# Kernel optimization log

Hardware: AMD Instinct MI355X
Metric: run time of the kernel (lower is better)

Reference implementation:

```python
import jax, jax.numpy as jnp
import numpy as np

B, T, OBS, ENC, H, A = 32, 512, 256, 1024, 1024, 64
AR_COEF, TAR_COEF = 0.01, 0.01
LN_EPS = 1e-5


def setup_inputs() -> dict:
    key = jax.random.key(0)
    ks = jax.random.split(key, 8)
    s = 0.02  # weight scale to keep activations in a sane range
    # PyTorch LSTM bias init in source: zeros, forget-gate slice [H:2H] = 1.0 (both b_ih and b_hh)
    b_gate = jnp.zeros((4 * H,), jnp.float32).at[H:2 * H].set(1.0)
    return {
        "obs": jax.random.normal(ks[0], (B, T, OBS), jnp.float32),
        "hxs": jnp.zeros((B, H), jnp.float32),
        "cxs": jnp.zeros((B, H), jnp.float32),
        "W1": jax.random.normal(ks[1], (ENC, OBS), jnp.float32) * s,
        "b1": jnp.zeros((ENC,), jnp.float32),
        "W2": jax.random.normal(ks[2], (ENC, ENC), jnp.float32) * s,
        "b2": jnp.zeros((ENC,), jnp.float32),
        "W_ih": jax.random.normal(ks[3], (4 * H, ENC), jnp.float32) * s,
        "W_hh": jax.random.normal(ks[4], (4 * H, H), jnp.float32) * s,
        "b_ih": b_gate,
        "b_hh": b_gate,
        "ln_g": jnp.ones((H,), jnp.float32),
        "ln_b": jnp.zeros((H,), jnp.float32),
        "Wa": jax.random.normal(ks[5], (A, H), jnp.float32) * s,
        "ba": jnp.zeros((A,), jnp.float32),
        "Wc": jax.random.normal(ks[6], (1, H), jnp.float32) * s,
        "bc": jnp.zeros((1,), jnp.float32),
    }


def reference(obs, hxs, cxs, W1, b1, W2, b2, W_ih, W_hh, b_ih, b_hh,
              ln_g, ln_b, Wa, ba, Wc, bc):
    # Encoder: Linear -> SiLU -> Linear -> SiLU
    enc = jax.nn.silu(obs @ W1.T + b1)
    enc = jax.nn.silu(enc @ W2.T + b2)  # (B,T,ENC)

    # LSTM (WeightDrop is identity in eval mode / p=0). Precompute input gates.
    gx = enc @ W_ih.T + (b_ih + b_hh)  # (B,T,4H)

    def step(carry, g_t):
        h, c = carry
        g = g_t + h @ W_hh.T  # (B,4H), PyTorch gate order: i, f, g, o
        i, f, gc, o = jnp.split(g, 4, axis=-1)
        c = jax.nn.sigmoid(f) * c + jax.nn.sigmoid(i) * jnp.tanh(gc)
        h = jax.nn.sigmoid(o) * jnp.tanh(c)
        return (h, c), h

    (h_n, c_n), hs = jax.lax.scan(step, (hxs, cxs), jnp.swapaxes(gx, 0, 1))
    out = jnp.swapaxes(hs, 0, 1)  # (B,T,H)

    # LayerNorm
    mu = out.mean(-1, keepdims=True)
    var = out.var(-1, keepdims=True)
    out = (out - mu) / jnp.sqrt(var + LN_EPS) * ln_g + ln_b

    ar_loss = jnp.mean(out ** 2) * AR_COEF
    tar_loss = jnp.mean((out[:, 1:, :] - out[:, :-1, :]) ** 2) * TAR_COEF

    logits = out @ Wa.T + ba          # (B,T,A)
    values = (out @ Wc.T + bc)[..., 0]  # (B,T)
    return logits, values, h_n, c_n, ar_loss, tar_loss
```

## Files before the change

kernel.cpp:

```cpp
#include <hip/hip_runtime.h>


typedef _Float16 half8 __attribute__((ext_vector_type(8)));
typedef _Float16 half4v __attribute__((ext_vector_type(4)));
typedef float floatx4 __attribute__((ext_vector_type(4)));
typedef unsigned long long ull;

__device__ __forceinline__ float sigmoidf_(float x) { return 1.f / (1.f + __expf(-x)); }
__device__ __forceinline__ float tanhf_(float x) {
  x = fminf(15.f, fmaxf(-15.f, x));
  float e = __expf(-2.f * x);
  return (1.f - e) / (1.f + e);
}

__global__ __launch_bounds__(256) void k_convert_all(
    const float* s0, _Float16* d0, int n0,
    const float* s1, _Float16* d1, int n1,
    const float* s2, _Float16* d2, int n2,
    const float* s3, _Float16* d3, int n3,
    const float* s4, _Float16* d4, int n4,
    const float* s5, _Float16* d5, int n5,
    const float* s6, _Float16* d6, int n6,
    const float* s7, _Float16* d7, int n7)
{
  const int gid = blockIdx.x * 256 + threadIdx.x;
  const int stride = gridDim.x * 256;
#define CONV_SEG(s, d, n)                                                  \
  for (int i = gid; i < (n); i += stride) {                                \
    floatx4 v = *(const floatx4*)((s) + (size_t)i * 4);                    \
    half4v h;                                                              \
    h[0] = (_Float16)v[0]; h[1] = (_Float16)v[1];                          \
    h[2] = (_Float16)v[2]; h[3] = (_Float16)v[3];                          \
    *(half4v*)((d) + (size_t)i * 4) = h;                                   \
  }
  CONV_SEG(s0, d0, n0)
  CONV_SEG(s1, d1, n1)
  CONV_SEG(s2, d2, n2)
  CONV_SEG(s3, d3, n3)
  CONV_SEG(s4, d4, n4)
  CONV_SEG(s5, d5, n5)
  CONV_SEG(s6, d6, n6)
  CONV_SEG(s7, d7, n7)
#undef CONV_SEG
}

template<int EPI>
__global__ __launch_bounds__(256) void k_gemm(
    const _Float16* __restrict__ A, const _Float16* __restrict__ B,
    _Float16* __restrict__ C, const float* __restrict__ bias0,
    const float* __restrict__ bias1, int M, int N, int K)
{
  __shared__ _Float16 As[128 * 32];
  __shared__ _Float16 Bs[128 * 32];
  const int tid = threadIdx.x;
  const int l = tid & 63;
  const int w = tid >> 6;
  const int wr = w >> 1, wc = w & 1;
  const _Float16* Ab = A + (size_t)blockIdx.x * 128 * K;
  const _Float16* Bb = B + (size_t)blockIdx.y * 128 * K;

  floatx4 acc[4][4];
#pragma unroll
  for (int a = 0; a < 4; ++a)
#pragma unroll
    for (int b = 0; b < 4; ++b) acc[a][b] = (floatx4){0.f, 0.f, 0.f, 0.f};

  const int ci0 = tid, ci1 = tid + 256;
  const int r0 = ci0 >> 2, r1 = ci1 >> 2;
  const int q0 = (ci0 & 3) ^ ((r0 >> 2) & 3);
  const int q1 = (ci1 & 3) ^ ((r1 >> 2) & 3);
  const int lr = l & 15;
  const int ko = l >> 4;
  const int nkt = K >> 5;

  for (int kt = 0; kt < nkt; ++kt) {
    const _Float16* Ak = Ab + kt * 32;
    const _Float16* Bk = Bb + kt * 32;
    uint4 va0 = *(const uint4*)(Ak + (size_t)r0 * K + q0 * 8);
    uint4 va1 = *(const uint4*)(Ak + (size_t)r1 * K + q1 * 8);
    uint4 vb0 = *(const uint4*)(Bk + (size_t)r0 * K + q0 * 8);
    uint4 vb1 = *(const uint4*)(Bk + (size_t)r1 * K + q1 * 8);
    __syncthreads();
    *(uint4*)(As + ci0 * 8) = va0;
    *(uint4*)(As + ci1 * 8) = va1;
    *(uint4*)(Bs + ci0 * 8) = vb0;
    *(uint4*)(Bs + ci1 * 8) = vb1;
    __syncthreads();
    half8 af[4], bf[4];
#pragma unroll
    for (int mr = 0; mr < 4; ++mr) {
      int row = wr * 64 + mr * 16 + lr;
      int cq = ko ^ ((row >> 2) & 3);
      af[mr] = *(const half8*)(As + row * 32 + cq * 8);
    }
#pragma unroll
    for (int nc = 0; nc < 4; ++nc) {
      int col = wc * 64 + nc * 16 + lr;
      int cq = ko ^ ((col >> 2) & 3);
      bf[nc] = *(const half8*)(Bs + col * 32 + cq * 8);
    }
#pragma unroll
    for (int mr = 0; mr < 4; ++mr)
#pragma unroll
      for (int nc = 0; nc < 4; ++nc)
        acc[mr][nc] = __builtin_amdgcn_mfma_f32_16x16x32_f16(af[mr], bf[nc], acc[mr][nc], 0, 0, 0);
  }

  const int lq = l >> 4;
#pragma unroll
  for (int nc = 0; nc < 4; ++nc) {
    int gcol = blockIdx.y * 128 + wc * 64 + nc * 16 + lr;
    float bia = bias0[gcol];
    if (EPI == 1) bia += bias1[gcol];
#pragma unroll
    for (int mr = 0; mr < 4; ++mr) {
      int grow = blockIdx.x * 128 + wr * 64 + mr * 16 + lq * 4;
#pragma unroll
      for (int i = 0; i < 4; ++i) {
        float v = acc[mr][nc][i] + bia;
        if (EPI == 0) v = v * sigmoidf_(v);
        C[(size_t)(grow + i) * N + gcol] = (_Float16)v;
      }
    }
  }
}

__global__ __launch_bounds__(256, 1) void k_scan(
    const _Float16* __restrict__ gx,
    const _Float16* __restrict__ Whh,
    const float* __restrict__ cxs,
    _Float16* __restrict__ hstate,
    int* __restrict__ flags,
    _Float16* __restrict__ outh,
    float* __restrict__ out_hn, float* __restrict__ out_cn)
{
  const int blk = blockIdx.x;
  const int hbase = blk * 16;
  const int tid = threadIdx.x, l = tid & 63, wq = tid >> 6;
  __shared__ float red[2][4][4][2][4][64];

  const int cc = l & 15, ko = l >> 4;

  half8 bfr[4][8];
#pragma unroll
  for (int q = 0; q < 4; ++q)
#pragma unroll
    for (int kk = 0; kk < 8; ++kk)
      bfr[q][kk] = *(const half8*)(Whh + (size_t)(q * 1024 + hbase + cc) * 1024
                                   + wq * 256 + kk * 32 + ko * 8);

  const int gb = tid >> 3, gc2 = tid & 7;
  float c0 = cxs[gb * 1024 + hbase + gc2 * 2 + 0];
  float c1 = cxs[gb * 1024 + hbase + gc2 * 2 + 1];
  const int gmt = gb >> 4, greg = gb & 3;
  const int lane0 = ((gb & 15) >> 2) * 16 + gc2 * 2;

  const int* myflag = flags + ((wq * 16 + (l & 15)) * 4 + (l >> 4)) * 16;
  int* ourflag = flags + (blk * 4 + wq) * 16;

  unsigned gxv[4];
#pragma unroll
  for (int q = 0; q < 4; ++q)
    gxv[q] = *(const unsigned*)(gx + (size_t)gb * 512 * 4096
                                + q * 1024 + hbase + gc2 * 2);

  for (int t = 0; t < 512; ++t) {
    if (t > 0) {
      int guard = 0;
      while (true) {
        int f = __hip_atomic_load(myflag, __ATOMIC_RELAXED, __HIP_MEMORY_SCOPE_AGENT);
        if (__all(f >= t)) break;
        if (++guard > (1 << 17)) break;
        __builtin_amdgcn_s_sleep(1);
      }
      asm volatile("" ::: "memory");
      __builtin_amdgcn_sched_barrier(0);
    }

    const _Float16* hcur = hstate + (size_t)(t & 1) * 32768;
    const ull* p0 = (const ull*)(hcur + cc * 1024 + wq * 256 + ko * 8);
    const ull* p1 = (const ull*)(hcur + (16 + cc) * 1024 + wq * 256 + ko * 8);
    ull ld0[16], ld1[16];
#pragma unroll
    for (int kk = 0; kk < 8; ++kk) {
      ld0[kk * 2 + 0] = __hip_atomic_load(p0 + kk * 8 + 0, __ATOMIC_RELAXED, __HIP_MEMORY_SCOPE_AGENT);
      ld0[kk * 2 + 1] = __hip_atomic_load(p0 + kk * 8 + 1, __ATOMIC_RELAXED, __HIP_MEMORY_SCOPE_AGENT);
      ld1[kk * 2 + 0] = __hip_atomic_load(p1 + kk * 8 + 0, __ATOMIC_RELAXED, __HIP_MEMORY_SCOPE_AGENT);
      ld1[kk * 2 + 1] = __hip_atomic_load(p1 + kk * 8 + 1, __ATOMIC_RELAXED, __HIP_MEMORY_SCOPE_AGENT);
    }

    floatx4 acc[4][2];
#pragma unroll
    for (int q = 0; q < 4; ++q) {
      acc[q][0] = (floatx4){0.f, 0.f, 0.f, 0.f};
      acc[q][1] = (floatx4){0.f, 0.f, 0.f, 0.f};
    }
#pragma unroll
    for (int kk = 0; kk < 8; ++kk) {
      union { ull u2[2]; half8 h; } a0, a1;
      a0.u2[0] = ld0[kk * 2 + 0]; a0.u2[1] = ld0[kk * 2 + 1];
      a1.u2[0] = ld1[kk * 2 + 0]; a1.u2[1] = ld1[kk * 2 + 1];
#pragma unroll
      for (int q = 0; q < 4; ++q) {
        acc[q][0] = __builtin_amdgcn_mfma_f32_16x16x32_f16(a0.h, bfr[q][kk], acc[q][0], 0, 0, 0);
        acc[q][1] = __builtin_amdgcn_mfma_f32_16x16x32_f16(a1.h, bfr[q][kk], acc[q][1], 0, 0, 0);
      }
    }
    const int pp = t & 1;
#pragma unroll
    for (int q = 0; q < 4; ++q)
#pragma unroll
      for (int mt = 0; mt < 2; ++mt)
#pragma unroll
        for (int i = 0; i < 4; ++i)
          red[pp][wq][q][mt][i][l] = acc[q][mt][i];
    asm volatile("s_waitcnt lgkmcnt(0)" ::: "memory");
    __builtin_amdgcn_s_barrier();
    __builtin_amdgcn_sched_barrier(0);

    float pre0[4], pre1[4];
#pragma unroll
    for (int q = 0; q < 4; ++q) {
      pre0[q] = red[pp][0][q][gmt][greg][lane0] + red[pp][1][q][gmt][greg][lane0]
              + red[pp][2][q][gmt][greg][lane0] + red[pp][3][q][gmt][greg][lane0];
      pre1[q] = red[pp][0][q][gmt][greg][lane0 + 1] + red[pp][1][q][gmt][greg][lane0 + 1]
              + red[pp][2][q][gmt][greg][lane0 + 1] + red[pp][3][q][gmt][greg][lane0 + 1];
    }
    union { unsigned u; _Float16 h[2]; } g0, g1, g2, g3;
    g0.u = gxv[0]; g1.u = gxv[1]; g2.u = gxv[2]; g3.u = gxv[3];

    float i0 = sigmoidf_(pre0[0] + (float)g0.h[0]);
    float f0 = sigmoidf_(pre0[1] + (float)g1.h[0]);
    float gg0 = tanhf_(pre0[2] + (float)g2.h[0]);
    float o0 = sigmoidf_(pre0[3] + (float)g3.h[0]);
    c0 = f0 * c0 + i0 * gg0;
    float h0 = o0 * tanhf_(c0);

    float i1 = sigmoidf_(pre1[0] + (float)g0.h[1]);
    float f1 = sigmoidf_(pre1[1] + (float)g1.h[1]);
    float gg1 = tanhf_(pre1[2] + (float)g2.h[1]);
    float o1 = sigmoidf_(pre1[3] + (float)g3.h[1]);
    c1 = f1 * c1 + i1 * gg1;
    float h1 = o1 * tanhf_(c1);

    union { _Float16 h[2]; unsigned u; } hp;
    hp.h[0] = (_Float16)h0; hp.h[1] = (_Float16)h1;

    __hip_atomic_store((unsigned*)(hstate + (size_t)((t + 1) & 1) * 32768
                                   + (size_t)gb * 1024 + hbase + gc2 * 2),
                       hp.u, __ATOMIC_RELAXED, __HIP_MEMORY_SCOPE_AGENT);
    asm volatile("s_waitcnt vmcnt(0)" ::: "memory");
    __builtin_amdgcn_sched_barrier(0);
    if (l == 0 && t < 511)
      __hip_atomic_store(ourflag, t + 1, __ATOMIC_RELAXED,
                         __HIP_MEMORY_SCOPE_AGENT);

    *(unsigned*)(outh + ((size_t)gb * 512 + t) * 1024 + hbase + gc2 * 2) = hp.u;
    if (t == 511) {
      float2 hv; hv.x = h0; hv.y = h1;
      float2 cv; cv.x = c0; cv.y = c1;
      *(float2*)(out_hn + gb * 1024 + hbase + gc2 * 2) = hv;
      *(float2*)(out_cn + gb * 1024 + hbase + gc2 * 2) = cv;
    } else {
#pragma unroll
      for (int q = 0; q < 4; ++q)
        gxv[q] = *(const unsigned*)(gx + ((size_t)gb * 512 + t + 1) * 4096
                                    + q * 1024 + hbase + gc2 * 2);
    }
    __builtin_amdgcn_sched_barrier(0);
  }
}

__global__ __launch_bounds__(256) void k_ln(
    const _Float16* __restrict__ x, const float* __restrict__ gam,
    const float* __restrict__ bet, _Float16* __restrict__ y,
    float* __restrict__ arpart)
{
  const int m = blockIdx.x;
  const int tid = threadIdx.x;
  const int w = tid >> 6, l = tid & 63;
  half4v v = *(const half4v*)(x + (size_t)m * 1024 + tid * 4);
  float xv[4]; float s = 0.f, ss = 0.f;
#pragma unroll
  for (int j = 0; j < 4; ++j) { xv[j] = (float)v[j]; s += xv[j]; ss += xv[j] * xv[j]; }
#pragma unroll
  for (int off = 32; off > 0; off >>= 1) { s += __shfl_xor(s, off, 64); ss += __shfl_xor(ss, off, 64); }
  __shared__ float sw[4], ssw[4], bcast[2];
  if (l == 0) { sw[w] = s; ssw[w] = ss; }
  __syncthreads();
  if (tid == 0) {
    float S = sw[0] + sw[1] + sw[2] + sw[3];
    float SS = ssw[0] + ssw[1] + ssw[2] + ssw[3];
    float mu = S * (1.f / 1024.f);
    float var = SS * (1.f / 1024.f) - mu * mu;
    bcast[0] = mu; bcast[1] = rsqrtf(var + 1e-5f);
  }
  __syncthreads();
  float mu = bcast[0], rstd = bcast[1];
  float part = 0.f; half4v o;
#pragma unroll
  for (int j = 0; j < 4; ++j) {
    float nv = (xv[j] - mu) * rstd * gam[tid * 4 + j] + bet[tid * 4 + j];
    o[j] = (_Float16)nv;
    part += nv * nv;
  }
  *(half4v*)(y + (size_t)m * 1024 + tid * 4) = o;
#pragma unroll
  for (int off = 32; off > 0; off >>= 1) part += __shfl_xor(part, off, 64);
  if (l == 0) sw[w] = part;
  __syncthreads();
  if (tid == 0) arpart[m] = sw[0] + sw[1] + sw[2] + sw[3];
}

__global__ __launch_bounds__(256) void k_tar(const _Float16* __restrict__ y, float* __restrict__ tarpart) {
  const int tid = threadIdx.x;
  int gid = blockIdx.x * 256 + tid;
  const int stride = gridDim.x * 256;
  const int TOT = 32 * 511 * 256;
  float s = 0.f;
  for (int v = gid; v < TOT; v += stride) {
    int b = v / (511 * 256);
    int r = v - b * (511 * 256);
    size_t base = (size_t)b * 512 * 1024 + (size_t)r * 4;
    half4v a = *(const half4v*)(y + base);
    half4v c = *(const half4v*)(y + base + 1024);
#pragma unroll
    for (int j = 0; j < 4; ++j) { float d = (float)c[j] - (float)a[j]; s += d * d; }
  }
#pragma unroll
  for (int off = 32; off > 0; off >>= 1) s += __shfl_xor(s, off, 64);
  __shared__ float sw[4];
  if ((tid & 63) == 0) sw[tid >> 6] = s;
  __syncthreads();
  if (tid == 0) tarpart[blockIdx.x] = sw[0] + sw[1] + sw[2] + sw[3];
}

__global__ __launch_bounds__(256) void k_reduce(
    const float* __restrict__ arpart, const float* __restrict__ tarpart,
    float* __restrict__ dst)
{
  const int tid = threadIdx.x;
  float a = 0.f, t = 0.f;
  for (int i = tid; i < 16384; i += 256) a += arpart[i];
  for (int i = tid; i < 2048; i += 256) t += tarpart[i];
#pragma unroll
  for (int off = 32; off > 0; off >>= 1) { a += __shfl_xor(a, off, 64); t += __shfl_xor(t, off, 64); }
  __shared__ float sa[4], st[4];
  if ((tid & 63) == 0) { sa[tid >> 6] = a; st[tid >> 6] = t; }
  __syncthreads();
  if (tid == 0) {
    dst[0] = (sa[0] + sa[1] + sa[2] + sa[3]) * (0.01f / 16777216.f);
    dst[1] = (st[0] + st[1] + st[2] + st[3]) * (0.01f / 16744448.f);
  }
}

__global__ __launch_bounds__(256) void k_logits(
    const _Float16* __restrict__ X, const _Float16* __restrict__ Wa,
    const float* __restrict__ ba, float* __restrict__ out)
{
  const int tid = threadIdx.x, l = tid & 63, w = tid >> 6;
  const int lr = l & 15, lq = l >> 4;
  const int rowb = blockIdx.x * 64 + w * 16;
  floatx4 acc[4];
#pragma unroll
  for (int nc = 0; nc < 4; ++nc) acc[nc] = (floatx4){0.f, 0.f, 0.f, 0.f};
  for (int kc = 0; kc < 32; ++kc) {
    int k = kc * 32 + lq * 8;
    half8 af = *(const half8*)(X + (size_t)(rowb + lr) * 1024 + k);
#pragma unroll
    for (int nc = 0; nc < 4; ++nc) {
      half8 bf = *(const half8*)(Wa + (size_t)(nc * 16 + lr) * 1024 + k);
      acc[nc] = __builtin_amdgcn_mfma_f32_16x16x32_f16(af, bf, acc[nc], 0, 0, 0);
    }
  }
#pragma unroll
  for (int nc = 0; nc < 4; ++nc) {
    int col = nc * 16 + lr;
    float bia = ba[col];
#pragma unroll
    for (int i = 0; i < 4; ++i) {
      int grow = rowb + lq * 4 + i;
      out[(size_t)grow * 64 + col] = acc[nc][i] + bia;
    }
  }
}

__global__ __launch_bounds__(256) void k_values(
    const _Float16* __restrict__ X, const _Float16* __restrict__ Wc,
    const float* __restrict__ bc, float* __restrict__ out)
{
  const int tid = threadIdx.x, l = tid & 63, w = tid >> 6;
  half8 w0 = *(const half8*)(Wc + l * 16);
  half8 w1 = *(const half8*)(Wc + l * 16 + 8);
  float bias = bc[0];
  const int rowb = blockIdx.x * 64 + w * 16;
  for (int r = 0; r < 16; ++r) {
    const _Float16* xr = X + (size_t)(rowb + r) * 1024 + l * 16;
    half8 x0 = *(const half8*)(xr);
    half8 x1 = *(const half8*)(xr + 8);
    float s = 0.f;
#pragma unroll
    for (int j = 0; j < 8; ++j) s += (float)x0[j] * (float)w0[j] + (float)x1[j] * (float)w1[j];
#pragma unroll
    for (int off = 32; off > 0; off >>= 1) s += __shfl_xor(s, off, 64);
    if (l == 0) out[rowb + r] = s + bias;
  }
}

extern "C" void kernel_launch(void* const* d_in, const int* in_sizes, int n_in,
                              void* d_out, int out_size, void* d_ws, size_t ws_size,
                              hipStream_t stream)
{
  const float* obs = (const float*)d_in[0];
  const float* hxs = (const float*)d_in[1];
  const float* cxs = (const float*)d_in[2];
  const float* W1  = (const float*)d_in[3];
  const float* b1  = (const float*)d_in[4];
  const float* W2  = (const float*)d_in[5];
  const float* b2  = (const float*)d_in[6];
  const float* Wih = (const float*)d_in[7];
  const float* Whh = (const float*)d_in[8];
  const float* bih = (const float*)d_in[9];
  const float* bhh = (const float*)d_in[10];
  const float* lng = (const float*)d_in[11];
  const float* lnb = (const float*)d_in[12];
  const float* Wa  = (const float*)d_in[13];
  const float* ba  = (const float*)d_in[14];
  const float* Wc  = (const float*)d_in[15];
  const float* bc  = (const float*)d_in[16];

  char* ws = (char*)d_ws;
  size_t off = 0;
  auto alloc = [&](size_t bytes) -> char* {
    char* p = ws + off;
    off += (bytes + 255) & ~(size_t)255;
    return p;
  };
  _Float16* obs16 = (_Float16*)alloc(4194304ull * 2);
  _Float16* W1x   = (_Float16*)alloc(262144ull * 2);
  _Float16* W2x   = (_Float16*)alloc(1048576ull * 2);
  _Float16* Wihx  = (_Float16*)alloc(4194304ull * 2);
  _Float16* Whhx  = (_Float16*)alloc(4194304ull * 2);
  _Float16* Wax   = (_Float16*)alloc(65536ull * 2);
  _Float16* Wcx   = (_Float16*)alloc(1024ull * 2);
  _Float16* enc1  = (_Float16*)alloc(16384ull * 1024 * 2);
  _Float16* enc2  = (_Float16*)alloc(16384ull * 1024 * 2);
  _Float16* gx    = (_Float16*)alloc(16384ull * 4096 * 2);
  _Float16* hstate= (_Float16*)alloc(2ull * 32 * 1024 * 2);
  int* flags      = (int*)alloc(64ull * 4 * 16 * 4);
  _Float16* outh  = (_Float16*)alloc(16384ull * 1024 * 2);
  float* arpart   = (float*)alloc(16384ull * 4);
  float* tarpart  = (float*)alloc(2048ull * 4);
  _Float16* normed = enc1;

  float* out_f      = (float*)d_out;
  float* out_logits = out_f;
  float* out_values = out_f + 1048576;
  float* out_hn     = out_f + 1064960;
  float* out_cn     = out_f + 1097728;
  float* out_loss   = out_f + 1130496;

  hipMemsetAsync(flags, 0, 64ull * 4 * 16 * 4, stream);

  k_convert_all<<<2048, 256, 0, stream>>>(
      obs, obs16, 4194304 / 4,
      W1, W1x, 262144 / 4,
      W2, W2x, 1048576 / 4,
      Wih, Wihx, 4194304 / 4,
      Whh, Whhx, 4194304 / 4,
      Wa, Wax, 65536 / 4,
      Wc, Wcx, 1024 / 4,
      hxs, hstate, 32768 / 4);

  k_gemm<0><<<dim3(128, 8), 256, 0, stream>>>(obs16, W1x, enc1, b1, nullptr, 16384, 1024, 256);
  k_gemm<0><<<dim3(128, 8), 256, 0, stream>>>(enc1, W2x, enc2, b2, nullptr, 16384, 1024, 1024);
  k_gemm<1><<<dim3(128, 32), 256, 0, stream>>>(enc2, Wihx, gx, bih, bhh, 16384, 4096, 1024);
  k_scan<<<64, 256, 0, stream>>>(gx, Whhx, cxs, hstate, flags, outh, out_hn, out_cn);
  k_ln<<<16384, 256, 0, stream>>>(outh, lng, lnb, normed, arpart);
  k_tar<<<2048, 256, 0, stream>>>(normed, tarpart);
  k_reduce<<<1, 256, 0, stream>>>(arpart, tarpart, out_loss);
  k_logits<<<256, 256, 0, stream>>>(normed, Wax, ba, out_logits);
  k_values<<<256, 256, 0, stream>>>(normed, Wcx, bc, out_values);
  (void)in_sizes; (void)n_in; (void)out_size; (void)ws_size;
}
```

Before: 3.428 ms.

## Fuse input-gate projection into persistent LSTM scan kernel

Removes the separate gx GEMM and its large fp16 intermediate buffer. Each scan block now keeps its slice of W_ih in registers alongside W_hh and computes enc2·W_ihᵀ for the current timestep before waiting on the cross-block flag, then adds the combined biases in the gate epilogue. This trades a bandwidth-heavy standalone GEMM plus gx reads for extra MFMA work and enc2 loads inside the serial loop, which only 64 blocks execute. It also roughly doubles register use for weight fragments, which could cause spills.

```diff
diff --git a/kernel.cpp b/kernel.cpp
--- a/kernel.cpp
+++ b/kernel.cpp
@@ -126,8 +126,10 @@
 }
 
 __global__ __launch_bounds__(256, 1) void k_scan(
-    const _Float16* __restrict__ gx,
+    const _Float16* __restrict__ enc2,
     const _Float16* __restrict__ Whh,
+    const _Float16* __restrict__ Wih,
+    const float* __restrict__ bih, const float* __restrict__ bhh,
     const float* __restrict__ cxs,
     _Float16* __restrict__ hstate,
     int* __restrict__ flags,
@@ -141,30 +143,66 @@
 
   const int cc = l & 15, ko = l >> 4;
 
-  half8 bfr[4][8];
+  half8 bfr[4][8], bfi[4][8];
 #pragma unroll
   for (int q = 0; q < 4; ++q)
 #pragma unroll
-    for (int kk = 0; kk < 8; ++kk)
-      bfr[q][kk] = *(const half8*)(Whh + (size_t)(q * 1024 + hbase + cc) * 1024
+    for (int kk = 0; kk < 8; ++kk) {
+      const ull* ph = (const ull*)(Whh + (size_t)(q * 1024 + hbase + cc) * 1024
                                    + wq * 256 + kk * 32 + ko * 8);
+      const ull* pi = (const ull*)(Wih + (size_t)(q * 1024 + hbase + cc) * 1024
+                                   + wq * 256 + kk * 32 + ko * 8);
+      union { ull u2[2]; half8 h; } uh, ui;
+      uh.u2[0] = __hip_atomic_load(ph + 0, __ATOMIC_RELAXED, __HIP_MEMORY_SCOPE_AGENT);
+      uh.u2[1] = __hip_atomic_load(ph + 1, __ATOMIC_RELAXED, __HIP_MEMORY_SCOPE_AGENT);
+      ui.u2[0] = __hip_atomic_load(pi + 0, __ATOMIC_RELAXED, __HIP_MEMORY_SCOPE_AGENT);
+      ui.u2[1] = __hip_atomic_load(pi + 1, __ATOMIC_RELAXED, __HIP_MEMORY_SCOPE_AGENT);
+      bfr[q][kk] = uh.h;
+      bfi[q][kk] = ui.h;
+    }
 
   const int gb = tid >> 3, gc2 = tid & 7;
   float c0 = cxs[gb * 1024 + hbase + gc2 * 2 + 0];
   float c1 = cxs[gb * 1024 + hbase + gc2 * 2 + 1];
   const int gmt = gb >> 4, greg = gb & 3;
   const int lane0 = ((gb & 15) >> 2) * 16 + gc2 * 2;
+  float bias0v[4], bias1v[4];
+#pragma unroll
+  for (int q = 0; q < 4; ++q) {
+    int col = q * 1024 + hbase + gc2 * 2;
+    bias0v[q] = bih[col] + bhh[col];
+    bias1v[q] = bih[col + 1] + bhh[col + 1];
+  }
 
   const int* myflag = flags + ((wq * 16 + (l & 15)) * 4 + (l >> 4)) * 16;
   int* ourflag = flags + (blk * 4 + wq) * 16;
 
-  unsigned gxv[4];
-#pragma unroll
-  for (int q = 0; q < 4; ++q)
-    gxv[q] = *(const unsigned*)(gx + (size_t)gb * 512 * 4096
-                                + q * 1024 + hbase + gc2 * 2);
-
   for (int t = 0; t < 512; ++t) {
+    const _Float16* e0p = enc2 + ((size_t)cc * 512 + t) * 1024 + wq * 256 + ko * 8;
+    const _Float16* e1p = enc2 + ((size_t)(16 + cc) * 512 + t) * 1024 + wq * 256 + ko * 8;
+    uint4 e0[8], e1[8];
+#pragma unroll
+    for (int kk = 0; kk < 8; ++kk) {
+      e0[kk] = *(const uint4*)(e0p + kk * 32);
+      e1[kk] = *(const uint4*)(e1p + kk * 32);
+    }
+    floatx4 acc[4][2];
+#pragma unroll
+    for (int q = 0; q < 4; ++q) {
+      acc[q][0] = (floatx4){0.f, 0.f, 0.f, 0.f};
+      acc[q][1] = (floatx4){0.f, 0.f, 0.f, 0.f};
+    }
+#pragma unroll
+    for (int kk = 0; kk < 8; ++kk) {
+      union { uint4 u; half8 h; } a0, a1;
+      a0.u = e0[kk]; a1.u = e1[kk];
+#pragma unroll
+      for (int q = 0; q < 4; ++q) {
+        acc[q][0] = __builtin_amdgcn_mfma_f32_16x16x32_f16(a0.h, bfi[q][kk], acc[q][0], 0, 0, 0);
+        acc[q][1] = __builtin_amdgcn_mfma_f32_16x16x32_f16(a1.h, bfi[q][kk], acc[q][1], 0, 0, 0);
+      }
+    }
+
     if (t > 0) {
       int guard = 0;
       while (true) {
@@ -188,13 +226,6 @@
       ld1[kk * 2 + 0] = __hip_atomic_load(p1 + kk * 8 + 0, __ATOMIC_RELAXED, __HIP_MEMORY_SCOPE_AGENT);
       ld1[kk * 2 + 1] = __hip_atomic_load(p1 + kk * 8 + 1, __ATOMIC_RELAXED, __HIP_MEMORY_SCOPE_AGENT);
     }
-
-    floatx4 acc[4][2];
-#pragma unroll
-    for (int q = 0; q < 4; ++q) {
-      acc[q][0] = (floatx4){0.f, 0.f, 0.f, 0.f};
-      acc[q][1] = (floatx4){0.f, 0.f, 0.f, 0.f};
-    }
 #pragma unroll
     for (int kk = 0; kk < 8; ++kk) {
       union { ull u2[2]; half8 h; } a0, a1;
@@ -222,24 +253,24 @@
 #pragma unroll
     for (int q = 0; q < 4; ++q) {
       pre0[q] = red[pp][0][q][gmt][greg][lane0] + red[pp][1][q][gmt][greg][lane0]
-              + red[pp][2][q][gmt][greg][lane0] + red[pp][3][q][gmt][greg][lane0];
+              + red[pp][2][q][gmt][greg][lane0] + red[pp][3][q][gmt][greg][lane0]
+              + bias0v[q];
       pre1[q] = red[pp][0][q][gmt][greg][lane0 + 1] + red[pp][1][q][gmt][greg][lane0 + 1]
-              + red[pp][2][q][gmt][greg][lane0 + 1] + red[pp][3][q][gmt][greg][lane0 + 1];
-    }
-    union { unsigned u; _Float16 h[2]; } g0, g1, g2, g3;
-    g0.u = gxv[0]; g1.u = gxv[1]; g2.u = gxv[2]; g3.u = gxv[3];
-
-    float i0 = sigmoidf_(pre0[0] + (float)g0.h[0]);
-    float f0 = sigmoidf_(pre0[1] + (float)g1.h[0]);
-    float gg0 = tanhf_(pre0[2] + (float)g2.h[0]);
-    float o0 = sigmoidf_(pre0[3] + (float)g3.h[0]);
+              + red[pp][2][q][gmt][greg][lane0 + 1] + red[pp][3][q][gmt][greg][lane0 + 1]
+              + bias1v[q];
+    }
+
+    float i0 = sigmoidf_(pre0[0]);
+    float f0 = sigmoidf_(pre0[1]);
+    float gg0 = tanhf_(pre0[2]);
+    float o0 = sigmoidf_(pre0[3]);
     c0 = f0 * c0 + i0 * gg0;
     float h0 = o0 * tanhf_(c0);
 
-    float i1 = sigmoidf_(pre1[0] + (float)g0.h[1]);
-    float f1 = sigmoidf_(pre1[1] + (float)g1.h[1]);
-    float gg1 = tanhf_(pre1[2] + (float)g2.h[1]);
-    float o1 = sigmoidf_(pre1[3] + (float)g3.h[1]);
+    float i1 = sigmoidf_(pre1[0]);
+    float f1 = sigmoidf_(pre1[1]);
+    float gg1 = tanhf_(pre1[2]);
+    float o1 = sigmoidf_(pre1[3]);
     c1 = f1 * c1 + i1 * gg1;
     float h1 = o1 * tanhf_(c1);
 
@@ -261,11 +292,6 @@
       float2 cv; cv.x = c0; cv.y = c1;
       *(float2*)(out_hn + gb * 1024 + hbase + gc2 * 2) = hv;
       *(float2*)(out_cn + gb * 1024 + hbase + gc2 * 2) = cv;
-    } else {
-#pragma unroll
-      for (int q = 0; q < 4; ++q)
-        gxv[q] = *(const unsigned*)(gx + ((size_t)gb * 512 + t + 1) * 4096
-                                    + q * 1024 + hbase + gc2 * 2);
     }
     __builtin_amdgcn_sched_barrier(0);
   }
@@ -445,7 +471,6 @@
   _Float16* Wcx   = (_Float16*)alloc(1024ull * 2);
   _Float16* enc1  = (_Float16*)alloc(16384ull * 1024 * 2);
   _Float16* enc2  = (_Float16*)alloc(16384ull * 1024 * 2);
-  _Float16* gx    = (_Float16*)alloc(16384ull * 4096 * 2);
   _Float16* hstate= (_Float16*)alloc(2ull * 32 * 1024 * 2);
   int* flags      = (int*)alloc(64ull * 4 * 16 * 4);
   _Float16* outh  = (_Float16*)alloc(16384ull * 1024 * 2);
@@ -474,8 +499,8 @@
 
   k_gemm<0><<<dim3(128, 8), 256, 0, stream>>>(obs16, W1x, enc1, b1, nullptr, 16384, 1024, 256);
   k_gemm<0><<<dim3(128, 8), 256, 0, stream>>>(enc1, W2x, enc2, b2, nullptr, 16384, 1024, 1024);
-  k_gemm<1><<<dim3(128, 32), 256, 0, stream>>>(enc2, Wihx, gx, bih, bhh, 16384, 4096, 1024);
-  k_scan<<<64, 256, 0, stream>>>(gx, Whhx, cxs, hstate, flags, outh, out_hn, out_cn);
+  k_scan<<<64, 256, 0, stream>>>(enc2, Whhx, Wihx, bih, bhh, cxs, hstate,
+                                 flags, outh, out_hn, out_cn);
   k_ln<<<16384, 256, 0, stream>>>(outh, lng, lnb, normed, arpart);
   k_tar<<<2048, 256, 0, stream>>>(normed, tarpart);
   k_reduce<<<1, 256, 0, stream>>>(arpart, tarpart, out_loss);
```

Result: slower. 4.305 ms (+25.6%).

## Tag recurrent hidden state with step counters to skip flag polling in LSTM scan

Applied to the files above, without the earlier changes.

Stores each fp16 pair of the hidden state together with a 32-bit timestep tag in one 64-bit word, so readers can check validity directly from the loaded data. The separate flag spin-wait runs only when some tag is stale, followed by a reload. The aim is to take the flag round-trip off the per-step critical path of the sequential scan. In exchange, each step loads twice as many bytes of hidden state, and an extra init kernel plus a memset are added.

```diff
diff --git a/kernel.cpp b/kernel.cpp
--- a/kernel.cpp
+++ b/kernel.cpp
@@ -20,8 +20,7 @@
     const float* s3, _Float16* d3, int n3,
     const float* s4, _Float16* d4, int n4,
     const float* s5, _Float16* d5, int n5,
-    const float* s6, _Float16* d6, int n6,
-    const float* s7, _Float16* d7, int n7)
+    const float* s6, _Float16* d6, int n6)
 {
   const int gid = blockIdx.x * 256 + threadIdx.x;
   const int stride = gridDim.x * 256;
@@ -40,8 +39,17 @@
   CONV_SEG(s4, d4, n4)
   CONV_SEG(s5, d5, n5)
   CONV_SEG(s6, d6, n6)
-  CONV_SEG(s7, d7, n7)
 #undef CONV_SEG
+}
+
+__global__ __launch_bounds__(256) void k_inith(const float* __restrict__ hxs,
+                                               ull* __restrict__ hT) {
+  int s = blockIdx.x * 256 + threadIdx.x;
+  int batch = s >> 9, pair = s & 511;
+  union { _Float16 h[2]; unsigned u; } p;
+  p.h[0] = (_Float16)hxs[batch * 1024 + pair * 2];
+  p.h[1] = (_Float16)hxs[batch * 1024 + pair * 2 + 1];
+  hT[s] = (ull)p.u | (1ull << 32);
 }
 
 template<int EPI>
@@ -129,7 +137,7 @@
     const _Float16* __restrict__ gx,
     const _Float16* __restrict__ Whh,
     const float* __restrict__ cxs,
-    _Float16* __restrict__ hstate,
+    ull* __restrict__ hT,
     int* __restrict__ flags,
     _Float16* __restrict__ outh,
     float* __restrict__ out_hn, float* __restrict__ out_cn)
@@ -165,7 +173,23 @@
                                 + q * 1024 + hbase + gc2 * 2);
 
   for (int t = 0; t < 512; ++t) {
-    if (t > 0) {
+    const ull* base0 = hT + (size_t)(t & 1) * 16384 + (size_t)cc * 512;
+    const ull* base1 = base0 + 16 * 512;
+    const unsigned tgt = (unsigned)(t + 1);
+    ull ld0[32], ld1[32];
+#pragma unroll
+    for (int kk = 0; kk < 8; ++kk)
+#pragma unroll
+      for (int j = 0; j < 4; ++j) {
+        int p = wq * 128 + kk * 16 + ko * 4 + j;
+        ld0[kk * 4 + j] = __hip_atomic_load(base0 + p, __ATOMIC_RELAXED, __HIP_MEMORY_SCOPE_AGENT);
+        ld1[kk * 4 + j] = __hip_atomic_load(base1 + p, __ATOMIC_RELAXED, __HIP_MEMORY_SCOPE_AGENT);
+      }
+    bool ok = true;
+#pragma unroll
+    for (int i = 0; i < 32; ++i)
+      ok &= ((unsigned)(ld0[i] >> 32) >= tgt) & ((unsigned)(ld1[i] >> 32) >= tgt);
+    if (!__all(ok)) {
       int guard = 0;
       while (true) {
         int f = __hip_atomic_load(myflag, __ATOMIC_RELAXED, __HIP_MEMORY_SCOPE_AGENT);
@@ -175,18 +199,14 @@
       }
       asm volatile("" ::: "memory");
       __builtin_amdgcn_sched_barrier(0);
-    }
-
-    const _Float16* hcur = hstate + (size_t)(t & 1) * 32768;
-    const ull* p0 = (const ull*)(hcur + cc * 1024 + wq * 256 + ko * 8);
-    const ull* p1 = (const ull*)(hcur + (16 + cc) * 1024 + wq * 256 + ko * 8);
-    ull ld0[16], ld1[16];
-#pragma unroll
-    for (int kk = 0; kk < 8; ++kk) {
-      ld0[kk * 2 + 0] = __hip_atomic_load(p0 + kk * 8 + 0, __ATOMIC_RELAXED, __HIP_MEMORY_SCOPE_AGENT);
-      ld0[kk * 2 + 1] = __hip_atomic_load(p0 + kk * 8 + 1, __ATOMIC_RELAXED, __HIP_MEMORY_SCOPE_AGENT);
-      ld1[kk * 2 + 0] = __hip_atomic_load(p1 + kk * 8 + 0, __ATOMIC_RELAXED, __HIP_MEMORY_SCOPE_AGENT);
-      ld1[kk * 2 + 1] = __hip_atomic_load(p1 + kk * 8 + 1, __ATOMIC_RELAXED, __HIP_MEMORY_SCOPE_AGENT);
+#pragma unroll
+      for (int kk = 0; kk < 8; ++kk)
+#pragma unroll
+        for (int j = 0; j < 4; ++j) {
+          int p = wq * 128 + kk * 16 + ko * 4 + j;
+          ld0[kk * 4 + j] = __hip_atomic_load(base0 + p, __ATOMIC_RELAXED, __HIP_MEMORY_SCOPE_AGENT);
+          ld1[kk * 4 + j] = __hip_atomic_load(base1 + p, __ATOMIC_RELAXED, __HIP_MEMORY_SCOPE_AGENT);
+        }
     }
 
     floatx4 acc[4][2];
@@ -197,9 +217,12 @@
     }
 #pragma unroll
     for (int kk = 0; kk < 8; ++kk) {
-      union { ull u2[2]; half8 h; } a0, a1;
-      a0.u2[0] = ld0[kk * 2 + 0]; a0.u2[1] = ld0[kk * 2 + 1];
-      a1.u2[0] = ld1[kk * 2 + 0]; a1.u2[1] = ld1[kk * 2 + 1];
+      union { unsigned u[4]; half8 h; } a0, a1;
+#pragma unroll
+      for (int j = 0; j < 4; ++j) {
+        a0.u[j] = (unsigned)ld0[kk * 4 + j];
+        a1.u[j] = (unsigned)ld1[kk * 4 + j];
+      }
 #pragma unroll
       for (int q = 0; q < 4; ++q) {
         acc[q][0] = __builtin_amdgcn_mfma_f32_16x16x32_f16(a0.h, bfr[q][kk], acc[q][0], 0, 0, 0);
@@ -246,9 +269,9 @@
     union { _Float16 h[2]; unsigned u; } hp;
     hp.h[0] = (_Float16)h0; hp.h[1] = (_Float16)h1;
 
-    __hip_atomic_store((unsigned*)(hstate + (size_t)((t + 1) & 1) * 32768
-                                   + (size_t)gb * 1024 + hbase + gc2 * 2),
-                       hp.u, __ATOMIC_RELAXED, __HIP_MEMORY_SCOPE_AGENT);
+    ull st = (ull)hp.u | ((ull)(unsigned)(t + 2) << 32);
+    __hip_atomic_store(hT + (size_t)((t + 1) & 1) * 16384 + gb * 512 + blk * 8 + gc2,
+                       st, __ATOMIC_RELAXED, __HIP_MEMORY_SCOPE_AGENT);
     asm volatile("s_waitcnt vmcnt(0)" ::: "memory");
     __builtin_amdgcn_sched_barrier(0);
     if (l == 0 && t < 511)
@@ -446,7 +469,7 @@
   _Float16* enc1  = (_Float16*)alloc(16384ull * 1024 * 2);
   _Float16* enc2  = (_Float16*)alloc(16384ull * 1024 * 2);
   _Float16* gx    = (_Float16*)alloc(16384ull * 4096 * 2);
-  _Float16* hstate= (_Float16*)alloc(2ull * 32 * 1024 * 2);
+  ull* hT         = (ull*)alloc(2ull * 16384 * 8);
   int* flags      = (int*)alloc(64ull * 4 * 16 * 4);
   _Float16* outh  = (_Float16*)alloc(16384ull * 1024 * 2);
   float* arpart   = (float*)alloc(16384ull * 4);
@@ -460,7 +483,9 @@
   float* out_cn     = out_f + 1097728;
   float* out_loss   = out_f + 1130496;
 
+  hipMemsetAsync(hT, 0, 2ull * 16384 * 8, stream);
   hipMemsetAsync(flags, 0, 64ull * 4 * 16 * 4, stream);
+  k_inith<<<64, 256, 0, stream>>>(hxs, hT);
 
   k_convert_all<<<2048, 256, 0, stream>>>(
       obs, obs16, 4194304 / 4,
@@ -469,13 +494,12 @@
       Wih, Wihx, 4194304 / 4,
       Whh, Whhx, 4194304 / 4,
       Wa, Wax, 65536 / 4,
-      Wc, Wcx, 1024 / 4,
-      hxs, hstate, 32768 / 4);
+      Wc, Wcx, 1024 / 4);
 
   k_gemm<0><<<dim3(128, 8), 256, 0, stream>>>(obs16, W1x, enc1, b1, nullptr, 16384, 1024, 256);
   k_gemm<0><<<dim3(128, 8), 256, 0, stream>>>(enc1, W2x, enc2, b2, nullptr, 16384, 1024, 1024);
   k_gemm<1><<<dim3(128, 32), 256, 0, stream>>>(enc2, Wihx, gx, bih, bhh, 16384, 4096, 1024);
-  k_scan<<<64, 256, 0, stream>>>(gx, Whhx, cxs, hstate, flags, outh, out_hn, out_cn);
+  k_scan<<<64, 256, 0, stream>>>(gx, Whhx, cxs, hT, flags, outh, out_hn, out_cn);
   k_ln<<<16384, 256, 0, stream>>>(outh, lng, lnb, normed, arpart);
   k_tar<<<2048, 256, 0, stream>>>(normed, tarpart);
   k_reduce<<<1, 256, 0, stream>>>(arpart, tarpart, out_loss);
```

New measurement: 7.173 ms. 109% more time.
